# Kernel tuning notes

Hardware: AMD Instinct MI355X
Metric: run time of the kernel (lower is better)

## Reference

```python
import jax, jax.numpy as jnp
import numpy as np


def gru_cell(x, h, wi, wh, bi, bh):
    # torch.nn.GRUCell math
    gi = x @ wi.T + bi  # (B, 3*H)
    gh = h @ wh.T + bh
    i_r, i_z, i_n = jnp.split(gi, 3, axis=-1)
    h_r, h_z, h_n = jnp.split(gh, 3, axis=-1)
    r = jax.nn.sigmoid(i_r + h_r)
    z = jax.nn.sigmoid(i_z + h_z)
    n = jnp.tanh(i_n + r * h_n)
    return (1.0 - z) * n + z * h


def setup_inputs() -> dict:
    key = jax.random.key(0)
    B, T = 256, 512
    dim_ctx, dim_mel, r = 512, 160, 2
    dim_pre, dim_att = 128, 256
    dim_rnn = dim_att + dim_ctx  # 768
    ks = jax.random.split(key, 32)
    rn = lambda k, shp, s=0.05: jax.random.normal(k, shp, jnp.float32) * s
    w = jax.random.uniform(ks[1], (B, T), jnp.float32)
    w = w / jnp.sum(w, axis=1, keepdims=True)  # valid attention distribution
    return {
        "x": rn(ks[0], (B, r, dim_mel // r), 1.0),
        "w": w,
        "h_att": jnp.zeros((B, dim_att), jnp.float32),
        "h_dec0": jnp.zeros((B, dim_rnn), jnp.float32),
        "h_dec1": jnp.zeros((B, dim_rnn), jnp.float32),
        "memory": rn(ks[2], (B, T, dim_ctx), 1.0),
        # PreNet: Linear(dim_mel->dim_pre)+ReLU, Linear(dim_pre->dim_pre)+ReLU
        "pre_w1": rn(ks[3], (dim_pre, dim_mel)), "pre_b1": rn(ks[4], (dim_pre,)),
        "pre_w2": rn(ks[5], (dim_pre, dim_pre)), "pre_b2": rn(ks[6], (dim_pre,)),
        # attention GRUCell (dim_pre -> dim_att)
        "att_wi": rn(ks[7], (3 * dim_att, dim_pre)), "att_wh": rn(ks[8], (3 * dim_att, dim_att)),
        "att_bi": rn(ks[9], (3 * dim_att,)), "att_bh": rn(ks[10], (3 * dim_att,)),
        # ContentMarkovAttention query projection (dim_att -> dim_ctx)
        "q_w": rn(ks[11], (dim_ctx, dim_att)), "q_b": rn(ks[12], (dim_ctx,)),
        # ResGRUCell 0 (dim_rnn -> dim_rnn)
        "dec0_wi": rn(ks[13], (3 * dim_rnn, dim_rnn)), "dec0_wh": rn(ks[14], (3 * dim_rnn, dim_rnn)),
        "dec0_bi": rn(ks[15], (3 * dim_rnn,)), "dec0_bh": rn(ks[16], (3 * dim_rnn,)),
        # ResGRUCell 1
        "dec1_wi": rn(ks[17], (3 * dim_rnn, dim_rnn)), "dec1_wh": rn(ks[18], (3 * dim_rnn, dim_rnn)),
        "dec1_bi": rn(ks[19], (3 * dim_rnn,)), "dec1_bh": rn(ks[20], (3 * dim_rnn,)),
    }


def reference(x, w, h_att, h_dec0, h_dec1, memory,
              pre_w1, pre_b1, pre_w2, pre_b2,
              att_wi, att_wh, att_bi, att_bh,
              q_w, q_b,
              dec0_wi, dec0_wh, dec0_bi, dec0_bh,
              dec1_wi, dec1_wh, dec1_bi, dec1_bh):
    B = x.shape[0]
    # PreNet on flattened r*mel frames
    xf = x.reshape(B, -1)
    h = jax.nn.relu(xf @ pre_w1.T + pre_b1)
    h = jax.nn.relu(h @ pre_w2.T + pre_b2)  # (B, dim_pre)
    # context vector with PREVIOUS attention weights (matches bmm before update)
    ctx = jnp.einsum('bt,btc->bc', w, memory)
    # attention GRU
    h_att_new = gru_cell(h, h_att, att_wi, att_wh, att_bi, att_bh)
    # ContentMarkovAttention: content scores * Markov (stay/move) prior, renormalized
    q = h_att_new @ q_w.T + q_b  # (B, dim_ctx)
    e = jnp.einsum('btc,bc->bt', memory, q) / jnp.sqrt(jnp.float32(memory.shape[-1]))
    a = jax.nn.softmax(e, axis=-1)
    w_shift = jnp.concatenate([jnp.zeros_like(w[:, :1]), w[:, :-1]], axis=1)
    w_prior = 0.5 * (w + w_shift)
    w_new = a * w_prior
    w_new = w_new / (jnp.sum(w_new, axis=1, keepdims=True) + 1e-8)
    # stacked residual GRU cells on [h_att; ctx]
    x_dec = jnp.concatenate([h_att_new, ctx], axis=1)  # (B, dim_rnn)
    h0 = gru_cell(x_dec, h_dec0, dec0_wi, dec0_wh, dec0_bi, dec0_bh) + x_dec
    h1 = gru_cell(h0, h_dec1, dec1_wi, dec1_wh, dec1_bi, dec1_bh) + h0
    return h1, w_new, h_att_new, h0, h1
```

## Files before the change

kernel.cpp:

```cpp
#include <hip/hip_runtime.h>
#include <math.h>

#define B    256
#define T    512
#define CTX  512
#define MEL  160
#define PRE  128
#define ATT  256
#define RNN  768
#define G3   2304

typedef __attribute__((ext_vector_type(8))) short short8;
typedef __attribute__((ext_vector_type(4))) float f32x4;

__device__ __forceinline__ unsigned short f2bf(float f) {
    unsigned u = __float_as_uint(f);
    unsigned r = (u + 0x7fffu + ((u >> 16) & 1u)) >> 16;
    return (unsigned short)r;
}
__device__ __forceinline__ float bf2f(unsigned short h) {
    return __uint_as_float((unsigned)h << 16);
}

__device__ __forceinline__ void conv8(const float* p, short8* hi8, short8* lo8) {
    const float4 v0 = *(const float4*)p;
    const float4 v1 = *(const float4*)(p + 4);
    const float av[8] = {v0.x, v0.y, v0.z, v0.w, v1.x, v1.y, v1.z, v1.w};
    short hi[8], lo[8];
    #pragma unroll
    for (int u = 0; u < 8; ++u) {
        const unsigned short h = f2bf(av[u]);
        hi[u] = (short)h;
        lo[u] = (short)f2bf(av[u] - bf2f(h));
    }
    *hi8 = *(const short8*)hi;
    *lo8 = *(const short8*)lo;
}

__global__ void wconv_kernel(const float* __restrict__ pw1, const float* __restrict__ pw2,
                             const float* __restrict__ wi, const float* __restrict__ wh,
                             const float* __restrict__ qw,
                             short* __restrict__ p1h, short* __restrict__ p1l,
                             short* __restrict__ p2h, short* __restrict__ p2l,
                             short* __restrict__ wih, short* __restrict__ wil,
                             short* __restrict__ whh, short* __restrict__ whl,
                             short* __restrict__ qwh, short* __restrict__ qwl) {
    int s = blockIdx.x * 256 + threadIdx.x;
    const float* src; short *dh, *dl; int K, KS, slot;
    if (s < 2560)                       { src = pw1; dh = p1h; dl = p1l; K = MEL; KS = 5; slot = s; }
    else if ((s -= 2560) < 2048)        { src = pw2; dh = p2h; dl = p2l; K = PRE; KS = 4; slot = s; }
    else if ((s -= 2048) < 12288)       { src = wi;  dh = wih; dl = wil; K = PRE; KS = 4; slot = s; }
    else if ((s -= 12288) < 24576)      { src = wh;  dh = whh; dl = whl; K = ATT; KS = 8; slot = s; }
    else if ((s -= 24576) < 16384)      { src = qw;  dh = qwh; dl = qwl; K = ATT; KS = 8; slot = s; }
    else return;
    const int lane = slot & 63;
    const int ks = (slot >> 6) % KS;
    const int nt = (slot >> 6) / KS;
    const int n = nt * 16 + (lane & 15);
    const int k = ks * 32 + (lane >> 4) * 8;
    conv8(src + (size_t)n * K + k, (short8*)(dh + (size_t)slot * 8), (short8*)(dl + (size_t)slot * 8));
}

__global__ __launch_bounds__(512) void front_mfma_kernel(
        const float* __restrict__ x, const float* __restrict__ b1,
        const float* __restrict__ b2, const float* __restrict__ h_att,
        const float* __restrict__ bi, const float* __restrict__ bh,
        const float* __restrict__ qb,
        const short* __restrict__ p1h, const short* __restrict__ p1l,
        const short* __restrict__ p2h, const short* __restrict__ p2l,
        const short* __restrict__ wih, const short* __restrict__ wil,
        const short* __restrict__ whh, const short* __restrict__ whl,
        const short* __restrict__ qwh, const short* __restrict__ qwl,
        float* __restrict__ h_att_out, float* __restrict__ x_dec,
        float* __restrict__ q) {
    __shared__ __align__(16) short AH[8][64][8];
    __shared__ __align__(16) short AL[8][64][8];
    __shared__ __align__(16) float S[16][RNN];
    __shared__ __align__(16) float S2[16][RNN];
    __shared__ __align__(16) float hs[16][ATT];

    const int tid = threadIdx.x;
    const int wave = tid >> 6, lane = tid & 63;
    const int mb = blockIdx.x * 16;
    const int col = lane & 15, rowq = lane >> 4;

    for (int i = tid; i < 16 * ATT; i += 512)
        hs[i >> 8][i & 255] = h_att[(size_t)(mb + (i >> 8)) * ATT + (i & 255)];
    if (tid < 320) {
        const int sub = tid >> 6, ln = tid & 63;
        const int row = ln & 15, kk = sub * 32 + (ln >> 4) * 8;
        conv8(x + (size_t)(mb + row) * MEL + kk, (short8*)AH[sub][ln], (short8*)AL[sub][ln]);
    }
    __syncthreads();

    {
        const int nt = wave;
        f32x4 acc = {0.f, 0.f, 0.f, 0.f};
        #pragma unroll
        for (int ks = 0; ks < 5; ++ks) {
            const short8 a_h = *(const short8*)AH[ks][lane];
            const short8 a_l = *(const short8*)AL[ks][lane];
            const size_t fo = ((size_t)(nt * 5 + ks) * 64 + lane) * 8;
            const short8 b_h = *(const short8*)(p1h + fo);
            const short8 b_l = *(const short8*)(p1l + fo);
            acc = __builtin_amdgcn_mfma_f32_16x16x32_bf16(a_h, b_h, acc, 0, 0, 0);
            acc = __builtin_amdgcn_mfma_f32_16x16x32_bf16(a_l, b_h, acc, 0, 0, 0);
            acc = __builtin_amdgcn_mfma_f32_16x16x32_bf16(a_h, b_l, acc, 0, 0, 0);
        }
        const int j = nt * 16 + col;
        const float bb = b1[j];
        #pragma unroll
        for (int r = 0; r < 4; ++r)
            S[rowq * 4 + r][j] = fmaxf(acc[r] + bb, 0.f);
    }
    __syncthreads();
    if (tid < 256) {
        const int sub = tid >> 6, ln = tid & 63;
        const int row = ln & 15, kk = sub * 32 + (ln >> 4) * 8;
        conv8(&S[row][kk], (short8*)AH[sub][ln], (short8*)AL[sub][ln]);
    }
    __syncthreads();

    {
        const int nt = wave;
        f32x4 acc = {0.f, 0.f, 0.f, 0.f};
        #pragma unroll
        for (int ks = 0; ks < 4; ++ks) {
            const short8 a_h = *(const short8*)AH[ks][lane];
            const short8 a_l = *(const short8*)AL[ks][lane];
            const size_t fo = ((size_t)(nt * 4 + ks) * 64 + lane) * 8;
            const short8 b_h = *(const short8*)(p2h + fo);
            const short8 b_l = *(const short8*)(p2l + fo);
            acc = __builtin_amdgcn_mfma_f32_16x16x32_bf16(a_h, b_h, acc, 0, 0, 0);
            acc = __builtin_amdgcn_mfma_f32_16x16x32_bf16(a_l, b_h, acc, 0, 0, 0);
            acc = __builtin_amdgcn_mfma_f32_16x16x32_bf16(a_h, b_l, acc, 0, 0, 0);
        }
        const int j = wave * 16 + col;
        const float bb = b2[j];
        #pragma unroll
        for (int r = 0; r < 4; ++r)
            S[rowq * 4 + r][j] = fmaxf(acc[r] + bb, 0.f);
    }
    __syncthreads();
    if (tid < 256) {
        const int sub = tid >> 6, ln = tid & 63;
        const int row = ln & 15, kk = sub * 32 + (ln >> 4) * 8;
        conv8(&S[row][kk], (short8*)AH[sub][ln], (short8*)AL[sub][ln]);
    }
    __syncthreads();

    for (int t = 0; t < 6; ++t) {
        const int nt = wave * 6 + t;
        f32x4 acc = {0.f, 0.f, 0.f, 0.f};
        #pragma unroll
        for (int ks = 0; ks < 4; ++ks) {
            const short8 a_h = *(const short8*)AH[ks][lane];
            const short8 a_l = *(const short8*)AL[ks][lane];
            const size_t fo = ((size_t)(nt * 4 + ks) * 64 + lane) * 8;
            const short8 b_h = *(const short8*)(wih + fo);
            const short8 b_l = *(const short8*)(wil + fo);
            acc = __builtin_amdgcn_mfma_f32_16x16x32_bf16(a_h, b_h, acc, 0, 0, 0);
            acc = __builtin_amdgcn_mfma_f32_16x16x32_bf16(a_l, b_h, acc, 0, 0, 0);
            acc = __builtin_amdgcn_mfma_f32_16x16x32_bf16(a_h, b_l, acc, 0, 0, 0);
        }
        const int j = nt * 16 + col;
        #pragma unroll
        for (int r = 0; r < 4; ++r) S[rowq * 4 + r][j] = acc[r];
    }
    __syncthreads();
    {
        const int sub = tid >> 6, ln = tid & 63;
        const int row = ln & 15, kk = sub * 32 + (ln >> 4) * 8;
        conv8(&hs[row][kk], (short8*)AH[sub][ln], (short8*)AL[sub][ln]);
    }
    __syncthreads();

    for (int t = 0; t < 6; ++t) {
        const int nt = wave * 6 + t;
        f32x4 acc = {0.f, 0.f, 0.f, 0.f};
        #pragma unroll
        for (int ks = 0; ks < 8; ++ks) {
            const short8 a_h = *(const short8*)AH[ks][lane];
            const short8 a_l = *(const short8*)AL[ks][lane];
            const size_t fo = ((size_t)(nt * 8 + ks) * 64 + lane) * 8;
            const short8 b_h = *(const short8*)(whh + fo);
            const short8 b_l = *(const short8*)(whl + fo);
            acc = __builtin_amdgcn_mfma_f32_16x16x32_bf16(a_h, b_h, acc, 0, 0, 0);
            acc = __builtin_amdgcn_mfma_f32_16x16x32_bf16(a_l, b_h, acc, 0, 0, 0);
            acc = __builtin_amdgcn_mfma_f32_16x16x32_bf16(a_h, b_l, acc, 0, 0, 0);
        }
        const int j = nt * 16 + col;
        #pragma unroll
        for (int r = 0; r < 4; ++r) S2[rowq * 4 + r][j] = acc[r];
    }
    __syncthreads();

    for (int e = tid; e < 16 * ATT; e += 512) {
        const int b = e >> 8, j = e & 255;
        const float ir = S[b][j] + bi[j];
        const float iz = S[b][ATT + j] + bi[ATT + j];
        const float in_ = S[b][2 * ATT + j] + bi[2 * ATT + j];
        const float hr = S2[b][j] + bh[j];
        const float hz = S2[b][ATT + j] + bh[ATT + j];
        const float hn = S2[b][2 * ATT + j] + bh[2 * ATT + j];
        const float r = 1.f / (1.f + expf(-(ir + hr)));
        const float z = 1.f / (1.f + expf(-(iz + hz)));
        const float n = tanhf(in_ + r * hn);
        const float hnew = (1.f - z) * n + z * hs[b][j];
        h_att_out[(size_t)(mb + b) * ATT + j] = hnew;
        x_dec[(size_t)(mb + b) * RNN + j] = hnew;
        hs[b][j] = hnew;
    }
    __syncthreads();
    {
        const int sub = tid >> 6, ln = tid & 63;
        const int row = ln & 15, kk = sub * 32 + (ln >> 4) * 8;
        conv8(&hs[row][kk], (short8*)AH[sub][ln], (short8*)AL[sub][ln]);
    }
    __syncthreads();

    for (int t = 0; t < 4; ++t) {
        const int nt = wave * 4 + t;
        f32x4 acc = {0.f, 0.f, 0.f, 0.f};
        #pragma unroll
        for (int ks = 0; ks < 8; ++ks) {
            const short8 a_h = *(const short8*)AH[ks][lane];
            const short8 a_l = *(const short8*)AL[ks][lane];
            const size_t fo = ((size_t)(nt * 8 + ks) * 64 + lane) * 8;
            const short8 b_h = *(const short8*)(qwh + fo);
            const short8 b_l = *(const short8*)(qwl + fo);
            acc = __builtin_amdgcn_mfma_f32_16x16x32_bf16(a_h, b_h, acc, 0, 0, 0);
            acc = __builtin_amdgcn_mfma_f32_16x16x32_bf16(a_l, b_h, acc, 0, 0, 0);
            acc = __builtin_amdgcn_mfma_f32_16x16x32_bf16(a_h, b_l, acc, 0, 0, 0);
        }
        const int j = nt * 16 + col;
        const float bb = qb[j];
        #pragma unroll
        for (int r = 0; r < 4; ++r)
            q[(size_t)(mb + rowq * 4 + r) * CTX + j] = acc[r] + bb;
    }
}

__global__ void mempass_kernel(const float* __restrict__ mem, const float* __restrict__ w,
                               const float* __restrict__ q, float* __restrict__ e,
                               float* __restrict__ ctx_part) {
    const int b = blockIdx.y, slice = blockIdx.x;
    const int tid = threadIdx.x;
    const int wave = tid >> 6, lane = tid & 63;
    __shared__ float qs[CTX];
    __shared__ float ctx_s[4][CTX];
    for (int i = tid; i < CTX; i += 256) qs[i] = q[(size_t)b * CTX + i];
    __syncthreads();

    const int c0 = lane * 4;
    const int c1 = 256 + lane * 4;
    const float q0 = qs[c0], q1 = qs[c0 + 1], q2 = qs[c0 + 2], q3 = qs[c0 + 3];
    const float q4 = qs[c1], q5 = qs[c1 + 1], q6 = qs[c1 + 2], q7 = qs[c1 + 3];

    const float* mb = mem + (size_t)b * T * CTX;
    float acc[8] = {0.f, 0.f, 0.f, 0.f, 0.f, 0.f, 0.f, 0.f};
    const float invs = 0.04419417382415922f;
    const int t0 = slice * 64 + wave * 16;

    #pragma unroll 4
    for (int i = 0; i < 16; ++i) {
        const int t = t0 + i;
        const float* row = mb + (size_t)t * CTX;
        const float4 m0 = *(const float4*)(row + c0);
        const float4 m1 = *(const float4*)(row + c1);
        const float wt = w[(size_t)b * T + t];
        float ep = m0.x * q0 + m0.y * q1 + m0.z * q2 + m0.w * q3
                 + m1.x * q4 + m1.y * q5 + m1.z * q6 + m1.w * q7;
        #pragma unroll
        for (int off = 32; off; off >>= 1) ep += __shfl_xor(ep, off);
        if (lane == 0) e[(size_t)b * T + t] = ep * invs;
        acc[0] += wt * m0.x; acc[1] += wt * m0.y; acc[2] += wt * m0.z; acc[3] += wt * m0.w;
        acc[4] += wt * m1.x; acc[5] += wt * m1.y; acc[6] += wt * m1.z; acc[7] += wt * m1.w;
    }
    ctx_s[wave][c0] = acc[0]; ctx_s[wave][c0 + 1] = acc[1]; ctx_s[wave][c0 + 2] = acc[2]; ctx_s[wave][c0 + 3] = acc[3];
    ctx_s[wave][c1] = acc[4]; ctx_s[wave][c1 + 1] = acc[5]; ctx_s[wave][c1 + 2] = acc[6]; ctx_s[wave][c1 + 3] = acc[7];
    __syncthreads();
    for (int c = tid; c < CTX; c += 256) {
        const float s = ctx_s[0][c] + ctx_s[1][c] + ctx_s[2][c] + ctx_s[3][c];
        ctx_part[((size_t)slice * B + b) * CTX + c] = s;
    }
}

__global__ void mid_kernel(const float* __restrict__ part, float* __restrict__ x_dec,
                           const float* __restrict__ e, const float* __restrict__ w,
                           float* __restrict__ w_new) {
    const int tid = threadIdx.x;
    if (blockIdx.x < 512) {
        const int idx = blockIdx.x * 256 + tid;
        const int b = idx >> 9, c = idx & 511;
        float s = 0.f;
        #pragma unroll
        for (int sl = 0; sl < 8; ++sl) s += part[((size_t)sl * B + b) * CTX + c];
        x_dec[(size_t)b * RNN + ATT + c] = s;
        return;
    }
    const int b = blockIdx.x - 512;
    const int lane = tid & 63, wv = tid >> 6;
    __shared__ float red[4];
    const float* eb = e + (size_t)b * T;
    const float* wb = w + (size_t)b * T;
    const float e0 = eb[tid], e1 = eb[tid + 256];

    float m = fmaxf(e0, e1);
    #pragma unroll
    for (int o = 32; o; o >>= 1) m = fmaxf(m, __shfl_xor(m, o));
    if (lane == 0) red[wv] = m;
    __syncthreads();
    m = fmaxf(fmaxf(red[0], red[1]), fmaxf(red[2], red[3]));
    __syncthreads();

    const float x0 = expf(e0 - m), x1 = expf(e1 - m);
    float s = x0 + x1;
    #pragma unroll
    for (int o = 32; o; o >>= 1) s += __shfl_xor(s, o);
    if (lane == 0) red[wv] = s;
    __syncthreads();
    s = red[0] + red[1] + red[2] + red[3];
    __syncthreads();

    const float p0 = 0.5f * (wb[tid] + (tid > 0 ? wb[tid - 1] : 0.f));
    const float p1 = 0.5f * (wb[tid + 256] + wb[tid + 255]);
    const float m0 = (x0 / s) * p0;
    const float m1 = (x1 / s) * p1;
    float s2 = m0 + m1;
    #pragma unroll
    for (int o = 32; o; o >>= 1) s2 += __shfl_xor(s2, o);
    if (lane == 0) red[wv] = s2;
    __syncthreads();
    s2 = red[0] + red[1] + red[2] + red[3];
    const float inv = 1.f / (s2 + 1e-8f);
    w_new[(size_t)b * T + tid] = m0 * inv;
    w_new[(size_t)b * T + tid + 256] = m1 * inv;
}

__global__ __launch_bounds__(256) void mfma_gemm_kernel(
        const float* __restrict__ Agi, const float* __restrict__ Agh,
        const float* __restrict__ Wgi, const float* __restrict__ Wgh,
        float* __restrict__ Cgi, float* __restrict__ Cgh) {
    const int mat = blockIdx.z;
    const float* __restrict__ A = mat ? Agh : Agi;
    const float* __restrict__ W = mat ? Wgh : Wgi;
    float* __restrict__ C = mat ? Cgh : Cgi;

    const int m0 = blockIdx.y * 64;
    const int n0 = blockIdx.x * 64;

    __shared__ __align__(16) short AH[4096];
    __shared__ __align__(16) short AL[4096];
    __shared__ __align__(16) short WH[4096];
    __shared__ __align__(16) short WL[4096];

    const int tid = threadIdx.x;
    const int lane = tid & 63;
    const int wave = tid >> 6;
    const int wm = wave >> 1, wn = wave & 1;

    f32x4 acc[2][2] = {{{0.f, 0.f, 0.f, 0.f}, {0.f, 0.f, 0.f, 0.f}},
                       {{0.f, 0.f, 0.f, 0.f}, {0.f, 0.f, 0.f, 0.f}}};

    for (int k0 = 0; k0 < RNN; k0 += 64) {
        #pragma unroll
        for (int si = 0; si < 2; ++si) {
            const int s = tid + si * 256;
            const int sub = s >> 6;
            const int ln = s & 63;
            const int row = (sub >> 1) * 16 + (ln & 15);
            const int kk = (sub & 1) * 32 + (ln >> 4) * 8;
            conv8(A + (size_t)(m0 + row) * RNN + k0 + kk,
                  (short8*)&AH[s * 8], (short8*)&AL[s * 8]);
            conv8(W + (size_t)(n0 + row) * RNN + k0 + kk,
                  (short8*)&WH[s * 8], (short8*)&WL[s * 8]);
        }
        __syncthreads();

        #pragma unroll
        for (int ks = 0; ks < 2; ++ks) {
            short8 ah[2], al[2], wh[2], wl[2];
            #pragma unroll
            for (int i = 0; i < 2; ++i) {
                const int asub = ((wm * 2 + i) * 2 + ks);
                ah[i] = *(const short8*)&AH[(asub * 64 + lane) * 8];
                al[i] = *(const short8*)&AL[(asub * 64 + lane) * 8];
                const int wsub = ((wn * 2 + i) * 2 + ks);
                wh[i] = *(const short8*)&WH[(wsub * 64 + lane) * 8];
                wl[i] = *(const short8*)&WL[(wsub * 64 + lane) * 8];
            }
            #pragma unroll
            for (int i = 0; i < 2; ++i)
                #pragma unroll
                for (int j = 0; j < 2; ++j) {
                    acc[i][j] = __builtin_amdgcn_mfma_f32_16x16x32_bf16(ah[i], wh[j], acc[i][j], 0, 0, 0);
                    acc[i][j] = __builtin_amdgcn_mfma_f32_16x16x32_bf16(al[i], wh[j], acc[i][j], 0, 0, 0);
                    acc[i][j] = __builtin_amdgcn_mfma_f32_16x16x32_bf16(ah[i], wl[j], acc[i][j], 0, 0, 0);
                }
        }
        __syncthreads();
    }

    const int rowq = lane >> 4, col = lane & 15;
    #pragma unroll
    for (int i = 0; i < 2; ++i)
        #pragma unroll
        for (int j = 0; j < 2; ++j) {
            const int rbase = m0 + wm * 32 + i * 16 + rowq * 4;
            const int cidx = n0 + wn * 32 + j * 16 + col;
            #pragma unroll
            for (int r = 0; r < 4; ++r)
                C[(size_t)(rbase + r) * G3 + cidx] = acc[i][j][r];
        }
}

__global__ void gru_res_kernel(const float* __restrict__ gi, const float* __restrict__ gh,
                               const float* __restrict__ x_in, const float* __restrict__ h_prev,
                               const float* __restrict__ bi, const float* __restrict__ bh,
                               float* __restrict__ out0, float* __restrict__ out1) {
    const int idx = blockIdx.x * 256 + threadIdx.x;
    const int b = idx / RNN, j = idx % RNN;
    const float* gib = gi + (size_t)b * G3;
    const float* ghb = gh + (size_t)b * G3;
    const float ir = gib[j] + bi[j];
    const float iz = gib[RNN + j] + bi[RNN + j];
    const float in_ = gib[2 * RNN + j] + bi[2 * RNN + j];
    const float hr = ghb[j] + bh[j];
    const float hz = ghb[RNN + j] + bh[RNN + j];
    const float hn = ghb[2 * RNN + j] + bh[2 * RNN + j];
    const float r = 1.f / (1.f + expf(-(ir + hr)));
    const float z = 1.f / (1.f + expf(-(iz + hz)));
    const float n = tanhf(in_ + r * hn);
    const float res = (1.f - z) * n + z * h_prev[idx] + x_in[idx];
    out0[idx] = res;
    if (out1) out1[idx] = res;
}

extern "C" void kernel_launch(void* const* d_in, const int* in_sizes, int n_in,
                              void* d_out, int out_size, void* d_ws, size_t ws_size,
                              hipStream_t stream) {
    const float* x       = (const float*)d_in[0];
    const float* w       = (const float*)d_in[1];
    const float* h_att   = (const float*)d_in[2];
    const float* h_dec0  = (const float*)d_in[3];
    const float* h_dec1  = (const float*)d_in[4];
    const float* memory  = (const float*)d_in[5];
    const float* pre_w1  = (const float*)d_in[6];
    const float* pre_b1  = (const float*)d_in[7];
    const float* pre_w2  = (const float*)d_in[8];
    const float* pre_b2  = (const float*)d_in[9];
    const float* att_wi  = (const float*)d_in[10];
    const float* att_wh  = (const float*)d_in[11];
    const float* att_bi  = (const float*)d_in[12];
    const float* att_bh  = (const float*)d_in[13];
    const float* q_w     = (const float*)d_in[14];
    const float* q_b     = (const float*)d_in[15];
    const float* dec0_wi = (const float*)d_in[16];
    const float* dec0_wh = (const float*)d_in[17];
    const float* dec0_bi = (const float*)d_in[18];
    const float* dec0_bh = (const float*)d_in[19];
    const float* dec1_wi = (const float*)d_in[20];
    const float* dec1_wh = (const float*)d_in[21];
    const float* dec1_bi = (const float*)d_in[22];
    const float* dec1_bh = (const float*)d_in[23];

    float* out = (float*)d_out;
    float* o_h1a = out;
    float* o_wn  = out + 196608;
    float* o_ha  = out + 327680;
    float* o_h0  = out + 393216;
    float* o_h1b = out + 589824;

    float* ws    = (float*)d_ws;
    float* q     = ws;
    float* e     = ws + 131072;
    float* x_dec = ws + 262144;
    float* ctxp  = ws + 458752;
    float* gi    = ws + 1507328;
    float* gh    = ws + 2097152;
    short* sb    = (short*)(ws + 2686976);
    short* p1h = sb;             short* p1l = sb + 20480;
    short* p2h = sb + 40960;     short* p2l = sb + 57344;
    short* wih = sb + 73728;     short* wil = sb + 172032;
    short* whh = sb + 270336;    short* whl = sb + 466944;
    short* qwh = sb + 663552;    short* qwl = sb + 794624;

    wconv_kernel<<<226, 256, 0, stream>>>(pre_w1, pre_w2, att_wi, att_wh, q_w,
                                          p1h, p1l, p2h, p2l, wih, wil, whh, whl, qwh, qwl);
    front_mfma_kernel<<<16, 512, 0, stream>>>(x, pre_b1, pre_b2, h_att, att_bi, att_bh, q_b,
                                              p1h, p1l, p2h, p2l, wih, wil, whh, whl, qwh, qwl,
                                              o_ha, x_dec, q);
    mempass_kernel<<<dim3(8, B), 256, 0, stream>>>(memory, w, q, e, ctxp);
    mid_kernel<<<768, 256, 0, stream>>>(ctxp, x_dec, e, w, o_wn);

    mfma_gemm_kernel<<<dim3(G3 / 64, B / 64, 2), 256, 0, stream>>>(
        x_dec, h_dec0, dec0_wi, dec0_wh, gi, gh);
    gru_res_kernel<<<768, 256, 0, stream>>>(gi, gh, x_dec, h_dec0, dec0_bi, dec0_bh, o_h0, nullptr);

    mfma_gemm_kernel<<<dim3(G3 / 64, B / 64, 2), 256, 0, stream>>>(
        o_h0, h_dec1, dec1_wi, dec1_wh, gi, gh);
    gru_res_kernel<<<768, 256, 0, stream>>>(gi, gh, o_h0, h_dec1, dec1_bi, dec1_bh, o_h1a, o_h1b);
}
```

Baseline: 161.9 us.

## Hoist hidden-state GEMMs into prep kernel and fuse attention into one kernel

```diff
diff --git a/kernel.cpp b/kernel.cpp
--- a/kernel.cpp
+++ b/kernel.cpp
@@ -37,325 +37,10 @@
     *lo8 = *(const short8*)lo;
 }
 
-__global__ void wconv_kernel(const float* __restrict__ pw1, const float* __restrict__ pw2,
-                             const float* __restrict__ wi, const float* __restrict__ wh,
-                             const float* __restrict__ qw,
-                             short* __restrict__ p1h, short* __restrict__ p1l,
-                             short* __restrict__ p2h, short* __restrict__ p2l,
-                             short* __restrict__ wih, short* __restrict__ wil,
-                             short* __restrict__ whh, short* __restrict__ whl,
-                             short* __restrict__ qwh, short* __restrict__ qwl) {
-    int s = blockIdx.x * 256 + threadIdx.x;
-    const float* src; short *dh, *dl; int K, KS, slot;
-    if (s < 2560)                       { src = pw1; dh = p1h; dl = p1l; K = MEL; KS = 5; slot = s; }
-    else if ((s -= 2560) < 2048)        { src = pw2; dh = p2h; dl = p2l; K = PRE; KS = 4; slot = s; }
-    else if ((s -= 2048) < 12288)       { src = wi;  dh = wih; dl = wil; K = PRE; KS = 4; slot = s; }
-    else if ((s -= 12288) < 24576)      { src = wh;  dh = whh; dl = whl; K = ATT; KS = 8; slot = s; }
-    else if ((s -= 24576) < 16384)      { src = qw;  dh = qwh; dl = qwl; K = ATT; KS = 8; slot = s; }
-    else return;
-    const int lane = slot & 63;
-    const int ks = (slot >> 6) % KS;
-    const int nt = (slot >> 6) / KS;
-    const int n = nt * 16 + (lane & 15);
-    const int k = ks * 32 + (lane >> 4) * 8;
-    conv8(src + (size_t)n * K + k, (short8*)(dh + (size_t)slot * 8), (short8*)(dl + (size_t)slot * 8));
-}
-
-__global__ __launch_bounds__(512) void front_mfma_kernel(
-        const float* __restrict__ x, const float* __restrict__ b1,
-        const float* __restrict__ b2, const float* __restrict__ h_att,
-        const float* __restrict__ bi, const float* __restrict__ bh,
-        const float* __restrict__ qb,
-        const short* __restrict__ p1h, const short* __restrict__ p1l,
-        const short* __restrict__ p2h, const short* __restrict__ p2l,
-        const short* __restrict__ wih, const short* __restrict__ wil,
-        const short* __restrict__ whh, const short* __restrict__ whl,
-        const short* __restrict__ qwh, const short* __restrict__ qwl,
-        float* __restrict__ h_att_out, float* __restrict__ x_dec,
-        float* __restrict__ q) {
-    __shared__ __align__(16) short AH[8][64][8];
-    __shared__ __align__(16) short AL[8][64][8];
-    __shared__ __align__(16) float S[16][RNN];
-    __shared__ __align__(16) float S2[16][RNN];
-    __shared__ __align__(16) float hs[16][ATT];
-
-    const int tid = threadIdx.x;
-    const int wave = tid >> 6, lane = tid & 63;
-    const int mb = blockIdx.x * 16;
-    const int col = lane & 15, rowq = lane >> 4;
-
-    for (int i = tid; i < 16 * ATT; i += 512)
-        hs[i >> 8][i & 255] = h_att[(size_t)(mb + (i >> 8)) * ATT + (i & 255)];
-    if (tid < 320) {
-        const int sub = tid >> 6, ln = tid & 63;
-        const int row = ln & 15, kk = sub * 32 + (ln >> 4) * 8;
-        conv8(x + (size_t)(mb + row) * MEL + kk, (short8*)AH[sub][ln], (short8*)AL[sub][ln]);
-    }
-    __syncthreads();
-
-    {
-        const int nt = wave;
-        f32x4 acc = {0.f, 0.f, 0.f, 0.f};
-        #pragma unroll
-        for (int ks = 0; ks < 5; ++ks) {
-            const short8 a_h = *(const short8*)AH[ks][lane];
-            const short8 a_l = *(const short8*)AL[ks][lane];
-            const size_t fo = ((size_t)(nt * 5 + ks) * 64 + lane) * 8;
-            const short8 b_h = *(const short8*)(p1h + fo);
-            const short8 b_l = *(const short8*)(p1l + fo);
-            acc = __builtin_amdgcn_mfma_f32_16x16x32_bf16(a_h, b_h, acc, 0, 0, 0);
-            acc = __builtin_amdgcn_mfma_f32_16x16x32_bf16(a_l, b_h, acc, 0, 0, 0);
-            acc = __builtin_amdgcn_mfma_f32_16x16x32_bf16(a_h, b_l, acc, 0, 0, 0);
-        }
-        const int j = nt * 16 + col;
-        const float bb = b1[j];
-        #pragma unroll
-        for (int r = 0; r < 4; ++r)
-            S[rowq * 4 + r][j] = fmaxf(acc[r] + bb, 0.f);
-    }
-    __syncthreads();
-    if (tid < 256) {
-        const int sub = tid >> 6, ln = tid & 63;
-        const int row = ln & 15, kk = sub * 32 + (ln >> 4) * 8;
-        conv8(&S[row][kk], (short8*)AH[sub][ln], (short8*)AL[sub][ln]);
-    }
-    __syncthreads();
-
-    {
-        const int nt = wave;
-        f32x4 acc = {0.f, 0.f, 0.f, 0.f};
-        #pragma unroll
-        for (int ks = 0; ks < 4; ++ks) {
-            const short8 a_h = *(const short8*)AH[ks][lane];
-            const short8 a_l = *(const short8*)AL[ks][lane];
-            const size_t fo = ((size_t)(nt * 4 + ks) * 64 + lane) * 8;
-            const short8 b_h = *(const short8*)(p2h + fo);
-            const short8 b_l = *(const short8*)(p2l + fo);
-            acc = __builtin_amdgcn_mfma_f32_16x16x32_bf16(a_h, b_h, acc, 0, 0, 0);
-            acc = __builtin_amdgcn_mfma_f32_16x16x32_bf16(a_l, b_h, acc, 0, 0, 0);
-            acc = __builtin_amdgcn_mfma_f32_16x16x32_bf16(a_h, b_l, acc, 0, 0, 0);
-        }
-        const int j = wave * 16 + col;
-        const float bb = b2[j];
-        #pragma unroll
-        for (int r = 0; r < 4; ++r)
-            S[rowq * 4 + r][j] = fmaxf(acc[r] + bb, 0.f);
-    }
-    __syncthreads();
-    if (tid < 256) {
-        const int sub = tid >> 6, ln = tid & 63;
-        const int row = ln & 15, kk = sub * 32 + (ln >> 4) * 8;
-        conv8(&S[row][kk], (short8*)AH[sub][ln], (short8*)AL[sub][ln]);
-    }
-    __syncthreads();
-
-    for (int t = 0; t < 6; ++t) {
-        const int nt = wave * 6 + t;
-        f32x4 acc = {0.f, 0.f, 0.f, 0.f};
-        #pragma unroll
-        for (int ks = 0; ks < 4; ++ks) {
-            const short8 a_h = *(const short8*)AH[ks][lane];
-            const short8 a_l = *(const short8*)AL[ks][lane];
-            const size_t fo = ((size_t)(nt * 4 + ks) * 64 + lane) * 8;
-            const short8 b_h = *(const short8*)(wih + fo);
-            const short8 b_l = *(const short8*)(wil + fo);
-            acc = __builtin_amdgcn_mfma_f32_16x16x32_bf16(a_h, b_h, acc, 0, 0, 0);
-            acc = __builtin_amdgcn_mfma_f32_16x16x32_bf16(a_l, b_h, acc, 0, 0, 0);
-            acc = __builtin_amdgcn_mfma_f32_16x16x32_bf16(a_h, b_l, acc, 0, 0, 0);
-        }
-        const int j = nt * 16 + col;
-        #pragma unroll
-        for (int r = 0; r < 4; ++r) S[rowq * 4 + r][j] = acc[r];
-    }
-    __syncthreads();
-    {
-        const int sub = tid >> 6, ln = tid & 63;
-        const int row = ln & 15, kk = sub * 32 + (ln >> 4) * 8;
-        conv8(&hs[row][kk], (short8*)AH[sub][ln], (short8*)AL[sub][ln]);
-    }
-    __syncthreads();
-
-    for (int t = 0; t < 6; ++t) {
-        const int nt = wave * 6 + t;
-        f32x4 acc = {0.f, 0.f, 0.f, 0.f};
-        #pragma unroll
-        for (int ks = 0; ks < 8; ++ks) {
-            const short8 a_h = *(const short8*)AH[ks][lane];
-            const short8 a_l = *(const short8*)AL[ks][lane];
-            const size_t fo = ((size_t)(nt * 8 + ks) * 64 + lane) * 8;
-            const short8 b_h = *(const short8*)(whh + fo);
-            const short8 b_l = *(const short8*)(whl + fo);
-            acc = __builtin_amdgcn_mfma_f32_16x16x32_bf16(a_h, b_h, acc, 0, 0, 0);
-            acc = __builtin_amdgcn_mfma_f32_16x16x32_bf16(a_l, b_h, acc, 0, 0, 0);
-            acc = __builtin_amdgcn_mfma_f32_16x16x32_bf16(a_h, b_l, acc, 0, 0, 0);
-        }
-        const int j = nt * 16 + col;
-        #pragma unroll
-        for (int r = 0; r < 4; ++r) S2[rowq * 4 + r][j] = acc[r];
-    }
-    __syncthreads();
-
-    for (int e = tid; e < 16 * ATT; e += 512) {
-        const int b = e >> 8, j = e & 255;
-        const float ir = S[b][j] + bi[j];
-        const float iz = S[b][ATT + j] + bi[ATT + j];
-        const float in_ = S[b][2 * ATT + j] + bi[2 * ATT + j];
-        const float hr = S2[b][j] + bh[j];
-        const float hz = S2[b][ATT + j] + bh[ATT + j];
-        const float hn = S2[b][2 * ATT + j] + bh[2 * ATT + j];
-        const float r = 1.f / (1.f + expf(-(ir + hr)));
-        const float z = 1.f / (1.f + expf(-(iz + hz)));
-        const float n = tanhf(in_ + r * hn);
-        const float hnew = (1.f - z) * n + z * hs[b][j];
-        h_att_out[(size_t)(mb + b) * ATT + j] = hnew;
-        x_dec[(size_t)(mb + b) * RNN + j] = hnew;
-        hs[b][j] = hnew;
-    }
-    __syncthreads();
-    {
-        const int sub = tid >> 6, ln = tid & 63;
-        const int row = ln & 15, kk = sub * 32 + (ln >> 4) * 8;
-        conv8(&hs[row][kk], (short8*)AH[sub][ln], (short8*)AL[sub][ln]);
-    }
-    __syncthreads();
-
-    for (int t = 0; t < 4; ++t) {
-        const int nt = wave * 4 + t;
-        f32x4 acc = {0.f, 0.f, 0.f, 0.f};
-        #pragma unroll
-        for (int ks = 0; ks < 8; ++ks) {
-            const short8 a_h = *(const short8*)AH[ks][lane];
-            const short8 a_l = *(const short8*)AL[ks][lane];
-            const size_t fo = ((size_t)(nt * 8 + ks) * 64 + lane) * 8;
-            const short8 b_h = *(const short8*)(qwh + fo);
-            const short8 b_l = *(const short8*)(qwl + fo);
-            acc = __builtin_amdgcn_mfma_f32_16x16x32_bf16(a_h, b_h, acc, 0, 0, 0);
-            acc = __builtin_amdgcn_mfma_f32_16x16x32_bf16(a_l, b_h, acc, 0, 0, 0);
-            acc = __builtin_amdgcn_mfma_f32_16x16x32_bf16(a_h, b_l, acc, 0, 0, 0);
-        }
-        const int j = nt * 16 + col;
-        const float bb = qb[j];
-        #pragma unroll
-        for (int r = 0; r < 4; ++r)
-            q[(size_t)(mb + rowq * 4 + r) * CTX + j] = acc[r] + bb;
-    }
-}
-
-__global__ void mempass_kernel(const float* __restrict__ mem, const float* __restrict__ w,
-                               const float* __restrict__ q, float* __restrict__ e,
-                               float* __restrict__ ctx_part) {
-    const int b = blockIdx.y, slice = blockIdx.x;
-    const int tid = threadIdx.x;
-    const int wave = tid >> 6, lane = tid & 63;
-    __shared__ float qs[CTX];
-    __shared__ float ctx_s[4][CTX];
-    for (int i = tid; i < CTX; i += 256) qs[i] = q[(size_t)b * CTX + i];
-    __syncthreads();
-
-    const int c0 = lane * 4;
-    const int c1 = 256 + lane * 4;
-    const float q0 = qs[c0], q1 = qs[c0 + 1], q2 = qs[c0 + 2], q3 = qs[c0 + 3];
-    const float q4 = qs[c1], q5 = qs[c1 + 1], q6 = qs[c1 + 2], q7 = qs[c1 + 3];
-
-    const float* mb = mem + (size_t)b * T * CTX;
-    float acc[8] = {0.f, 0.f, 0.f, 0.f, 0.f, 0.f, 0.f, 0.f};
-    const float invs = 0.04419417382415922f;
-    const int t0 = slice * 64 + wave * 16;
-
-    #pragma unroll 4
-    for (int i = 0; i < 16; ++i) {
-        const int t = t0 + i;
-        const float* row = mb + (size_t)t * CTX;
-        const float4 m0 = *(const float4*)(row + c0);
-        const float4 m1 = *(const float4*)(row + c1);
-        const float wt = w[(size_t)b * T + t];
-        float ep = m0.x * q0 + m0.y * q1 + m0.z * q2 + m0.w * q3
-                 + m1.x * q4 + m1.y * q5 + m1.z * q6 + m1.w * q7;
-        #pragma unroll
-        for (int off = 32; off; off >>= 1) ep += __shfl_xor(ep, off);
-        if (lane == 0) e[(size_t)b * T + t] = ep * invs;
-        acc[0] += wt * m0.x; acc[1] += wt * m0.y; acc[2] += wt * m0.z; acc[3] += wt * m0.w;
-        acc[4] += wt * m1.x; acc[5] += wt * m1.y; acc[6] += wt * m1.z; acc[7] += wt * m1.w;
-    }
-    ctx_s[wave][c0] = acc[0]; ctx_s[wave][c0 + 1] = acc[1]; ctx_s[wave][c0 + 2] = acc[2]; ctx_s[wave][c0 + 3] = acc[3];
-    ctx_s[wave][c1] = acc[4]; ctx_s[wave][c1 + 1] = acc[5]; ctx_s[wave][c1 + 2] = acc[6]; ctx_s[wave][c1 + 3] = acc[7];
-    __syncthreads();
-    for (int c = tid; c < CTX; c += 256) {
-        const float s = ctx_s[0][c] + ctx_s[1][c] + ctx_s[2][c] + ctx_s[3][c];
-        ctx_part[((size_t)slice * B + b) * CTX + c] = s;
-    }
-}
-
-__global__ void mid_kernel(const float* __restrict__ part, float* __restrict__ x_dec,
-                           const float* __restrict__ e, const float* __restrict__ w,
-                           float* __restrict__ w_new) {
-    const int tid = threadIdx.x;
-    if (blockIdx.x < 512) {
-        const int idx = blockIdx.x * 256 + tid;
-        const int b = idx >> 9, c = idx & 511;
-        float s = 0.f;
-        #pragma unroll
-        for (int sl = 0; sl < 8; ++sl) s += part[((size_t)sl * B + b) * CTX + c];
-        x_dec[(size_t)b * RNN + ATT + c] = s;
-        return;
-    }
-    const int b = blockIdx.x - 512;
-    const int lane = tid & 63, wv = tid >> 6;
-    __shared__ float red[4];
-    const float* eb = e + (size_t)b * T;
-    const float* wb = w + (size_t)b * T;
-    const float e0 = eb[tid], e1 = eb[tid + 256];
-
-    float m = fmaxf(e0, e1);
-    #pragma unroll
-    for (int o = 32; o; o >>= 1) m = fmaxf(m, __shfl_xor(m, o));
-    if (lane == 0) red[wv] = m;
-    __syncthreads();
-    m = fmaxf(fmaxf(red[0], red[1]), fmaxf(red[2], red[3]));
-    __syncthreads();
-
-    const float x0 = expf(e0 - m), x1 = expf(e1 - m);
-    float s = x0 + x1;
-    #pragma unroll
-    for (int o = 32; o; o >>= 1) s += __shfl_xor(s, o);
-    if (lane == 0) red[wv] = s;
-    __syncthreads();
-    s = red[0] + red[1] + red[2] + red[3];
-    __syncthreads();
-
-    const float p0 = 0.5f * (wb[tid] + (tid > 0 ? wb[tid - 1] : 0.f));
-    const float p1 = 0.5f * (wb[tid + 256] + wb[tid + 255]);
-    const float m0 = (x0 / s) * p0;
-    const float m1 = (x1 / s) * p1;
-    float s2 = m0 + m1;
-    #pragma unroll
-    for (int o = 32; o; o >>= 1) s2 += __shfl_xor(s2, o);
-    if (lane == 0) red[wv] = s2;
-    __syncthreads();
-    s2 = red[0] + red[1] + red[2] + red[3];
-    const float inv = 1.f / (s2 + 1e-8f);
-    w_new[(size_t)b * T + tid] = m0 * inv;
-    w_new[(size_t)b * T + tid + 256] = m1 * inv;
-}
-
-__global__ __launch_bounds__(256) void mfma_gemm_kernel(
-        const float* __restrict__ Agi, const float* __restrict__ Agh,
-        const float* __restrict__ Wgi, const float* __restrict__ Wgh,
-        float* __restrict__ Cgi, float* __restrict__ Cgh) {
-    const int mat = blockIdx.z;
-    const float* __restrict__ A = mat ? Agh : Agi;
-    const float* __restrict__ W = mat ? Wgh : Wgi;
-    float* __restrict__ C = mat ? Cgh : Cgi;
-
-    const int m0 = blockIdx.y * 64;
-    const int n0 = blockIdx.x * 64;
-
-    __shared__ __align__(16) short AH[4096];
-    __shared__ __align__(16) short AL[4096];
-    __shared__ __align__(16) short WH[4096];
-    __shared__ __align__(16) short WL[4096];
-
-    const int tid = threadIdx.x;
+__device__ __forceinline__ void gemm64_body(
+        const float* __restrict__ A, const float* __restrict__ W,
+        float* __restrict__ C, int m0, int n0, int tid,
+        short* AH, short* AL, short* WH, short* WL) {
     const int lane = tid & 63;
     const int wave = tid >> 6;
     const int wm = wave >> 1, wn = wave & 1;
@@ -413,6 +98,327 @@
             for (int r = 0; r < 4; ++r)
                 C[(size_t)(rbase + r) * G3 + cidx] = acc[i][j][r];
         }
+}
+
+__global__ __launch_bounds__(256) void prep_kernel(
+        const float* __restrict__ pw1, const float* __restrict__ pw2,
+        const float* __restrict__ wi, const float* __restrict__ wh,
+        const float* __restrict__ qw,
+        short* __restrict__ p1h, short* __restrict__ p1l,
+        short* __restrict__ p2h, short* __restrict__ p2l,
+        short* __restrict__ wih, short* __restrict__ wil,
+        short* __restrict__ whh, short* __restrict__ whl,
+        short* __restrict__ qwh, short* __restrict__ qwl,
+        const float* __restrict__ h_dec0, const float* __restrict__ dec0_wh,
+        const float* __restrict__ h_dec1, const float* __restrict__ dec1_wh,
+        float* __restrict__ gh0, float* __restrict__ gh1) {
+    __shared__ __align__(16) short AH[4096];
+    __shared__ __align__(16) short AL[4096];
+    __shared__ __align__(16) short WH[4096];
+    __shared__ __align__(16) short WL[4096];
+    const int blk = blockIdx.x;
+    const int tid = threadIdx.x;
+
+    if (blk < 226) {
+        int s = blk * 256 + tid;
+        const float* src; short *dh, *dl; int K, KS, slot;
+        if (s < 2560)                  { src = pw1; dh = p1h; dl = p1l; K = MEL; KS = 5; slot = s; }
+        else if ((s -= 2560) < 2048)   { src = pw2; dh = p2h; dl = p2l; K = PRE; KS = 4; slot = s; }
+        else if ((s -= 2048) < 12288)  { src = wi;  dh = wih; dl = wil; K = PRE; KS = 4; slot = s; }
+        else if ((s -= 12288) < 24576) { src = wh;  dh = whh; dl = whl; K = ATT; KS = 8; slot = s; }
+        else if ((s -= 24576) < 16384) { src = qw;  dh = qwh; dl = qwl; K = ATT; KS = 8; slot = s; }
+        else return;
+        const int lane = slot & 63;
+        const int ks = (slot >> 6) % KS;
+        const int nt = (slot >> 6) / KS;
+        const int n = nt * 16 + (lane & 15);
+        const int k = ks * 32 + (lane >> 4) * 8;
+        conv8(src + (size_t)n * K + k,
+              (short8*)(dh + (size_t)slot * 8), (short8*)(dl + (size_t)slot * 8));
+        return;
+    }
+    const int u = blk - 226;
+    const float* A; const float* W; float* C;
+    int r;
+    if (u < 144) { A = h_dec0; W = dec0_wh; C = gh0; r = u; }
+    else         { A = h_dec1; W = dec1_wh; C = gh1; r = u - 144; }
+    gemm64_body(A, W, C, (r / 36) * 64, (r % 36) * 64, tid, AH, AL, WH, WL);
+}
+
+__global__ __launch_bounds__(512) void front_mfma_kernel(
+        const float* __restrict__ x, const float* __restrict__ b1,
+        const float* __restrict__ b2, const float* __restrict__ h_att,
+        const float* __restrict__ bi, const float* __restrict__ bh,
+        const float* __restrict__ qb,
+        const short* __restrict__ p1h, const short* __restrict__ p1l,
+        const short* __restrict__ p2h, const short* __restrict__ p2l,
+        const short* __restrict__ wih, const short* __restrict__ wil,
+        const short* __restrict__ whh, const short* __restrict__ whl,
+        const short* __restrict__ qwh, const short* __restrict__ qwl,
+        float* __restrict__ h_att_out, float* __restrict__ x_dec,
+        float* __restrict__ q) {
+    __shared__ __align__(16) short AH[8][64][8];
+    __shared__ __align__(16) short AL[8][64][8];
+    __shared__ __align__(16) float S[16][RNN];
+    __shared__ __align__(16) float S2[16][RNN];
+    __shared__ __align__(16) float hs[16][ATT];
+
+    const int tid = threadIdx.x;
+    const int wave = tid >> 6, lane = tid & 63;
+    const int mb = blockIdx.x * 16;
+    const int col = lane & 15, rowq = lane >> 4;
+
+    for (int i = tid; i < 16 * ATT; i += 512)
+        hs[i >> 8][i & 255] = h_att[(size_t)(mb + (i >> 8)) * ATT + (i & 255)];
+    if (tid < 320) {
+        const int sub = tid >> 6, ln = tid & 63;
+        const int row = ln & 15, kk = sub * 32 + (ln >> 4) * 8;
+        conv8(x + (size_t)(mb + row) * MEL + kk, (short8*)AH[sub][ln], (short8*)AL[sub][ln]);
+    }
+    __syncthreads();
+
+    {
+        const int nt = wave;
+        f32x4 acc = {0.f, 0.f, 0.f, 0.f};
+        #pragma unroll
+        for (int ks = 0; ks < 5; ++ks) {
+            const short8 a_h = *(const short8*)AH[ks][lane];
+            const short8 a_l = *(const short8*)AL[ks][lane];
+            const size_t fo = ((size_t)(nt * 5 + ks) * 64 + lane) * 8;
+            const short8 b_h = *(const short8*)(p1h + fo);
+            const short8 b_l = *(const short8*)(p1l + fo);
+            acc = __builtin_amdgcn_mfma_f32_16x16x32_bf16(a_h, b_h, acc, 0, 0, 0);
+            acc = __builtin_amdgcn_mfma_f32_16x16x32_bf16(a_l, b_h, acc, 0, 0, 0);
+            acc = __builtin_amdgcn_mfma_f32_16x16x32_bf16(a_h, b_l, acc, 0, 0, 0);
+        }
+        const int j = nt * 16 + col;
+        const float bb = b1[j];
+        #pragma unroll
+        for (int r = 0; r < 4; ++r)
+            S[rowq * 4 + r][j] = fmaxf(acc[r] + bb, 0.f);
+    }
+    __syncthreads();
+    if (tid < 256) {
+        const int sub = tid >> 6, ln = tid & 63;
+        const int row = ln & 15, kk = sub * 32 + (ln >> 4) * 8;
+        conv8(&S[row][kk], (short8*)AH[sub][ln], (short8*)AL[sub][ln]);
+    }
+    __syncthreads();
+
+    {
+        const int nt = wave;
+        f32x4 acc = {0.f, 0.f, 0.f, 0.f};
+        #pragma unroll
+        for (int ks = 0; ks < 4; ++ks) {
+            const short8 a_h = *(const short8*)AH[ks][lane];
+            const short8 a_l = *(const short8*)AL[ks][lane];
+            const size_t fo = ((size_t)(nt * 4 + ks) * 64 + lane) * 8;
+            const short8 b_h = *(const short8*)(p2h + fo);
+            const short8 b_l = *(const short8*)(p2l + fo);
+            acc = __builtin_amdgcn_mfma_f32_16x16x32_bf16(a_h, b_h, acc, 0, 0, 0);
+            acc = __builtin_amdgcn_mfma_f32_16x16x32_bf16(a_l, b_h, acc, 0, 0, 0);
+            acc = __builtin_amdgcn_mfma_f32_16x16x32_bf16(a_h, b_l, acc, 0, 0, 0);
+        }
+        const int j = wave * 16 + col;
+        const float bb = b2[j];
+        #pragma unroll
+        for (int r = 0; r < 4; ++r)
+            S[rowq * 4 + r][j] = fmaxf(acc[r] + bb, 0.f);
+    }
+    __syncthreads();
+    if (tid < 256) {
+        const int sub = tid >> 6, ln = tid & 63;
+        const int row = ln & 15, kk = sub * 32 + (ln >> 4) * 8;
+        conv8(&S[row][kk], (short8*)AH[sub][ln], (short8*)AL[sub][ln]);
+    }
+    __syncthreads();
+
+    for (int t = 0; t < 6; ++t) {
+        const int nt = wave * 6 + t;
+        f32x4 acc = {0.f, 0.f, 0.f, 0.f};
+        #pragma unroll
+        for (int ks = 0; ks < 4; ++ks) {
+            const short8 a_h = *(const short8*)AH[ks][lane];
+            const short8 a_l = *(const short8*)AL[ks][lane];
+            const size_t fo = ((size_t)(nt * 4 + ks) * 64 + lane) * 8;
+            const short8 b_h = *(const short8*)(wih + fo);
+            const short8 b_l = *(const short8*)(wil + fo);
+            acc = __builtin_amdgcn_mfma_f32_16x16x32_bf16(a_h, b_h, acc, 0, 0, 0);
+            acc = __builtin_amdgcn_mfma_f32_16x16x32_bf16(a_l, b_h, acc, 0, 0, 0);
+            acc = __builtin_amdgcn_mfma_f32_16x16x32_bf16(a_h, b_l, acc, 0, 0, 0);
+        }
+        const int j = nt * 16 + col;
+        #pragma unroll
+        for (int r = 0; r < 4; ++r) S[rowq * 4 + r][j] = acc[r];
+    }
+    __syncthreads();
+    {
+        const int sub = tid >> 6, ln = tid & 63;
+        const int row = ln & 15, kk = sub * 32 + (ln >> 4) * 8;
+        conv8(&hs[row][kk], (short8*)AH[sub][ln], (short8*)AL[sub][ln]);
+    }
+    __syncthreads();
+
+    for (int t = 0; t < 6; ++t) {
+        const int nt = wave * 6 + t;
+        f32x4 acc = {0.f, 0.f, 0.f, 0.f};
+        #pragma unroll
+        for (int ks = 0; ks < 8; ++ks) {
+            const short8 a_h = *(const short8*)AH[ks][lane];
+            const short8 a_l = *(const short8*)AL[ks][lane];
+            const size_t fo = ((size_t)(nt * 8 + ks) * 64 + lane) * 8;
+            const short8 b_h = *(const short8*)(whh + fo);
+            const short8 b_l = *(const short8*)(whl + fo);
+            acc = __builtin_amdgcn_mfma_f32_16x16x32_bf16(a_h, b_h, acc, 0, 0, 0);
+            acc = __builtin_amdgcn_mfma_f32_16x16x32_bf16(a_l, b_h, acc, 0, 0, 0);
+            acc = __builtin_amdgcn_mfma_f32_16x16x32_bf16(a_h, b_l, acc, 0, 0, 0);
+        }
+        const int j = nt * 16 + col;
+        #pragma unroll
+        for (int r = 0; r < 4; ++r) S2[rowq * 4 + r][j] = acc[r];
+    }
+    __syncthreads();
+
+    for (int e = tid; e < 16 * ATT; e += 512) {
+        const int b = e >> 8, j = e & 255;
+        const float ir = S[b][j] + bi[j];
+        const float iz = S[b][ATT + j] + bi[ATT + j];
+        const float in_ = S[b][2 * ATT + j] + bi[2 * ATT + j];
+        const float hr = S2[b][j] + bh[j];
+        const float hz = S2[b][ATT + j] + bh[ATT + j];
+        const float hn = S2[b][2 * ATT + j] + bh[2 * ATT + j];
+        const float r = 1.f / (1.f + expf(-(ir + hr)));
+        const float z = 1.f / (1.f + expf(-(iz + hz)));
+        const float n = tanhf(in_ + r * hn);
+        const float hnew = (1.f - z) * n + z * hs[b][j];
+        h_att_out[(size_t)(mb + b) * ATT + j] = hnew;
+        x_dec[(size_t)(mb + b) * RNN + j] = hnew;
+        hs[b][j] = hnew;
+    }
+    __syncthreads();
+    {
+        const int sub = tid >> 6, ln = tid & 63;
+        const int row = ln & 15, kk = sub * 32 + (ln >> 4) * 8;
+        conv8(&hs[row][kk], (short8*)AH[sub][ln], (short8*)AL[sub][ln]);
+    }
+    __syncthreads();
+
+    for (int t = 0; t < 4; ++t) {
+        const int nt = wave * 4 + t;
+        f32x4 acc = {0.f, 0.f, 0.f, 0.f};
+        #pragma unroll
+        for (int ks = 0; ks < 8; ++ks) {
+            const short8 a_h = *(const short8*)AH[ks][lane];
+            const short8 a_l = *(const short8*)AL[ks][lane];
+            const size_t fo = ((size_t)(nt * 8 + ks) * 64 + lane) * 8;
+            const short8 b_h = *(const short8*)(qwh + fo);
+            const short8 b_l = *(const short8*)(qwl + fo);
+            acc = __builtin_amdgcn_mfma_f32_16x16x32_bf16(a_h, b_h, acc, 0, 0, 0);
+            acc = __builtin_amdgcn_mfma_f32_16x16x32_bf16(a_l, b_h, acc, 0, 0, 0);
+            acc = __builtin_amdgcn_mfma_f32_16x16x32_bf16(a_h, b_l, acc, 0, 0, 0);
+        }
+        const int j = nt * 16 + col;
+        const float bb = qb[j];
+        #pragma unroll
+        for (int r = 0; r < 4; ++r)
+            q[(size_t)(mb + rowq * 4 + r) * CTX + j] = acc[r] + bb;
+    }
+}
+
+__global__ __launch_bounds__(512) void attn_kernel(
+        const float* __restrict__ mem, const float* __restrict__ w,
+        const float* __restrict__ q, float* __restrict__ x_dec,
+        float* __restrict__ w_new) {
+    __shared__ float qs[CTX];
+    __shared__ float ws_[T];
+    __shared__ float e_s[T];
+    __shared__ float ctx_s[8][CTX];
+    __shared__ float red[8];
+
+    const int b = blockIdx.x;
+    const int tid = threadIdx.x;
+    const int wave = tid >> 6, lane = tid & 63;
+
+    if (tid < CTX) qs[tid] = q[(size_t)b * CTX + tid];
+    ws_[tid] = w[(size_t)b * T + tid];
+    __syncthreads();
+
+    const int c0 = lane * 4;
+    const int c1 = 256 + lane * 4;
+    const float q0 = qs[c0], q1 = qs[c0 + 1], q2 = qs[c0 + 2], q3 = qs[c0 + 3];
+    const float q4 = qs[c1], q5 = qs[c1 + 1], q6 = qs[c1 + 2], q7 = qs[c1 + 3];
+
+    const float* mb = mem + (size_t)b * T * CTX;
+    float acc[8] = {0.f, 0.f, 0.f, 0.f, 0.f, 0.f, 0.f, 0.f};
+    const float invs = 0.04419417382415922f;
+    const int t0 = wave * 64;
+
+    #pragma unroll 4
+    for (int i = 0; i < 64; ++i) {
+        const int t = t0 + i;
+        const float* row = mb + (size_t)t * CTX;
+        const float4 m0 = *(const float4*)(row + c0);
+        const float4 m1 = *(const float4*)(row + c1);
+        const float wt = ws_[t];
+        float ep = m0.x * q0 + m0.y * q1 + m0.z * q2 + m0.w * q3
+                 + m1.x * q4 + m1.y * q5 + m1.z * q6 + m1.w * q7;
+        #pragma unroll
+        for (int off = 32; off; off >>= 1) ep += __shfl_xor(ep, off);
+        if (lane == 0) e_s[t] = ep * invs;
+        acc[0] += wt * m0.x; acc[1] += wt * m0.y; acc[2] += wt * m0.z; acc[3] += wt * m0.w;
+        acc[4] += wt * m1.x; acc[5] += wt * m1.y; acc[6] += wt * m1.z; acc[7] += wt * m1.w;
+    }
+    ctx_s[wave][c0] = acc[0]; ctx_s[wave][c0 + 1] = acc[1]; ctx_s[wave][c0 + 2] = acc[2]; ctx_s[wave][c0 + 3] = acc[3];
+    ctx_s[wave][c1] = acc[4]; ctx_s[wave][c1 + 1] = acc[5]; ctx_s[wave][c1 + 2] = acc[6]; ctx_s[wave][c1 + 3] = acc[7];
+    __syncthreads();
+
+    {
+        const int c = tid;
+        float s = 0.f;
+        #pragma unroll
+        for (int wv = 0; wv < 8; ++wv) s += ctx_s[wv][c];
+        x_dec[(size_t)b * RNN + ATT + c] = s;
+    }
+
+    const float ev = e_s[tid];
+    float m = ev;
+    #pragma unroll
+    for (int o = 32; o; o >>= 1) m = fmaxf(m, __shfl_xor(m, o));
+    if (lane == 0) red[wave] = m;
+    __syncthreads();
+    m = red[0];
+    #pragma unroll
+    for (int wv = 1; wv < 8; ++wv) m = fmaxf(m, red[wv]);
+    __syncthreads();
+
+    const float x0 = expf(ev - m);
+    float s = x0;
+    #pragma unroll
+    for (int o = 32; o; o >>= 1) s += __shfl_xor(s, o);
+    if (lane == 0) red[wave] = s;
+    __syncthreads();
+    s = red[0] + red[1] + red[2] + red[3] + red[4] + red[5] + red[6] + red[7];
+    __syncthreads();
+
+    const float p = 0.5f * (ws_[tid] + (tid > 0 ? ws_[tid - 1] : 0.f));
+    const float m0v = (x0 / s) * p;
+    float s2 = m0v;
+    #pragma unroll
+    for (int o = 32; o; o >>= 1) s2 += __shfl_xor(s2, o);
+    if (lane == 0) red[wave] = s2;
+    __syncthreads();
+    s2 = red[0] + red[1] + red[2] + red[3] + red[4] + red[5] + red[6] + red[7];
+    w_new[(size_t)b * T + tid] = m0v / (s2 + 1e-8f);
+}
+
+__global__ __launch_bounds__(256) void gemm_gi_kernel(
+        const float* __restrict__ A, const float* __restrict__ W,
+        float* __restrict__ C) {
+    __shared__ __align__(16) short AH[4096];
+    __shared__ __align__(16) short AL[4096];
+    __shared__ __align__(16) short WH[4096];
+    __shared__ __align__(16) short WL[4096];
+    gemm64_body(A, W, C, blockIdx.y * 64, blockIdx.x * 64, threadIdx.x, AH, AL, WH, WL);
 }
 
 __global__ void gru_res_kernel(const float* __restrict__ gi, const float* __restrict__ gh,
@@ -474,31 +480,28 @@
 
     float* ws    = (float*)d_ws;
     float* q     = ws;
-    float* e     = ws + 131072;
-    float* x_dec = ws + 262144;
-    float* ctxp  = ws + 458752;
-    float* gi    = ws + 1507328;
-    float* gh    = ws + 2097152;
-    short* sb    = (short*)(ws + 2686976);
+    float* x_dec = ws + 131072;
+    float* gi    = ws + 327680;
+    float* gh0   = ws + 917504;
+    float* gh1   = ws + 1507328;
+    short* sb    = (short*)(ws + 2097152);
     short* p1h = sb;             short* p1l = sb + 20480;
     short* p2h = sb + 40960;     short* p2l = sb + 57344;
     short* wih = sb + 73728;     short* wil = sb + 172032;
     short* whh = sb + 270336;    short* whl = sb + 466944;
     short* qwh = sb + 663552;    short* qwl = sb + 794624;
 
-    wconv_kernel<<<226, 256, 0, stream>>>(pre_w1, pre_w2, att_wi, att_wh, q_w,
-                                          p1h, p1l, p2h, p2l, wih, wil, whh, whl, qwh, qwl);
+    prep_kernel<<<514, 256, 0, stream>>>(pre_w1, pre_w2, att_wi, att_wh, q_w,
+                                         p1h, p1l, p2h, p2l, wih, wil, whh, whl, qwh, qwl,
+                                         h_dec0, dec0_wh, h_dec1, dec1_wh, gh0, gh1);
     front_mfma_kernel<<<16, 512, 0, stream>>>(x, pre_b1, pre_b2, h_att, att_bi, att_bh, q_b,
                                               p1h, p1l, p2h, p2l, wih, wil, whh, whl, qwh, qwl,
                                               o_ha, x_dec, q);
-    mempass_kernel<<<dim3(8, B), 256, 0, stream>>>(memory, w, q, e, ctxp);
-    mid_kernel<<<768, 256, 0, stream>>>(ctxp, x_dec, e, w, o_wn);
-
-    mfma_gemm_kernel<<<dim3(G3 / 64, B / 64, 2), 256, 0, stream>>>(
-        x_dec, h_dec0, dec0_wi, dec0_wh, gi, gh);
-    gru_res_kernel<<<768, 256, 0, stream>>>(gi, gh, x_dec, h_dec0, dec0_bi, dec0_bh, o_h0, nullptr);
-
-    mfma_gemm_kernel<<<dim3(G3 / 64, B / 64, 2), 256, 0, stream>>>(
-        o_h0, h_dec1, dec1_wi, dec1_wh, gi, gh);
-    gru_res_kernel<<<768, 256, 0, stream>>>(gi, gh, o_h0, h_dec1, dec1_bi, dec1_bh, o_h1a, o_h1b);
-}
+    attn_kernel<<<B, 512, 0, stream>>>(memory, w, q, x_dec, o_wn);
+
+    gemm_gi_kernel<<<dim3(36, 4), 256, 0, stream>>>(x_dec, dec0_wi, gi);
+    gru_res_kernel<<<768, 256, 0, stream>>>(gi, gh0, x_dec, h_dec0, dec0_bi, dec0_bh, o_h0, nullptr);
+
+    gemm_gi_kernel<<<dim3(36, 4), 256, 0, stream>>>(o_h0, dec1_wi, gi);
+    gru_res_kernel<<<768, 256, 0, stream>>>(gi, gh1, o_h0, h_dec1, dec1_bi, dec1_bh, o_h1a, o_h1b);
+}
```

New measurement: 192.2 us. 1.19x slower.
